# Performance work log

Hardware: AMD Instinct MI355X
Metric: run time of the kernel (lower is better)

Reference implementation:

```python
import math
import jax, jax.numpy as jnp
import numpy as np

TAU = 2.0
THR = 1.0
ALPHA = 10.0

T, B, IN_DIM, OUT_DIM = 64, 128, 2048, 2048


def setup_inputs() -> dict:
    key = jax.random.key(0)
    k1, k2, k3 = jax.random.split(key, 3)
    x_seq = jax.random.normal(k1, (T, B, IN_DIM), dtype=jnp.float32)
    # scale like nn.Linear default init so membrane potentials are O(1)
    W = jax.random.normal(k2, (OUT_DIM, IN_DIM), dtype=jnp.float32) / math.sqrt(IN_DIM)
    b = jax.random.normal(k3, (OUT_DIM,), dtype=jnp.float32) * 0.01
    return {"x_seq": x_seq, "W": W, "b": b}


def spike(x):
    # forward: hard threshold (surrogate gradient only matters in bwd)
    return (x > 0).astype(x.dtype)


def reference(x_seq, W, b):
    decay = math.exp(-1.0 / TAU)
    # hoist the linear layer out of the recurrence: one big GEMM
    cur_seq = jnp.einsum("tbi,oi->tbo", x_seq, W) + b  # (T, B, OUT_DIM)
    mem0 = jnp.zeros((x_seq.shape[1], W.shape[0]), dtype=x_seq.dtype)

    def step(mem, cur):
        mem = mem * decay + cur
        spk = spike(mem - THR)
        mem = mem - spk * THR
        return mem, spk

    _, spk_seq = jax.lax.scan(step, mem0, cur_seq)
    return spk_seq  # (T, B, OUT_DIM)
```

## Files before the change

kernel.cpp:

```cpp
#include <hip/hip_runtime.h>
#include <hip/hip_bf16.h>
#include <math.h>


typedef unsigned short u16;
typedef __attribute__((ext_vector_type(8))) short bf16x8;
typedef __attribute__((ext_vector_type(4))) float f32x4;

constexpr int T_STEPS = 64;
constexpr int BATCH   = 128;
constexpr int K_DIM   = 2048;
constexpr int N_DIM   = 2048;
constexpr int M_DIM   = T_STEPS * BATCH;
constexpr int NCHAIN  = BATCH * N_DIM;

constexpr float DECAY_F32 = (float)0.6065306597126334;
constexpr float BAND      = 2e-4f;

#define GLDS16(g, l) __builtin_amdgcn_global_load_lds(                       \
    (const __attribute__((address_space(1))) void*)(g),                      \
    (__attribute__((address_space(3))) void*)(l), 16, 0, 0)

__global__ __launch_bounds__(256)
void split_bf16(const float* __restrict__ X, const float* __restrict__ W,
                u16* __restrict__ Ah, u16* __restrict__ Al,
                u16* __restrict__ Wh, u16* __restrict__ Wl,
                unsigned int* __restrict__ counters) {
    if (blockIdx.x == 0 && threadIdx.x < 128) counters[threadIdx.x] = 0u;

    constexpr int NA8 = (M_DIM * K_DIM) / 8;
    constexpr int NW8 = (N_DIM * K_DIM) / 8;
    const int i = blockIdx.x * 256 + threadIdx.x;
    const float* src; u16* dh; u16* dl; int base;
    if (i < NA8)            { src = X; dh = Ah; dl = Al; base = i; }
    else if (i < NA8 + NW8) { src = W; dh = Wh; dl = Wl; base = i - NA8; }
    else return;

    const float4 v0 = *(const float4*)(src + (size_t)base * 8);
    const float4 v1 = *(const float4*)(src + (size_t)base * 8 + 4);
    const float f[8] = {v0.x, v0.y, v0.z, v0.w, v1.x, v1.y, v1.z, v1.w};
    unsigned int hp[4], lp[4];
#pragma unroll
    for (int q = 0; q < 8; q += 2) {
        u16 hh[2], ll[2];
#pragma unroll
        for (int e = 0; e < 2; e++) {
            __hip_bfloat16 hb = __float2bfloat16(f[q + e]);
            const float hf = __bfloat162float(hb);
            __hip_bfloat16 lb = __float2bfloat16(f[q + e] - hf);
            hh[e] = *(u16*)&hb;
            ll[e] = *(u16*)&lb;
        }
        hp[q >> 1] = (unsigned int)hh[0] | ((unsigned int)hh[1] << 16);
        lp[q >> 1] = (unsigned int)ll[0] | ((unsigned int)ll[1] << 16);
    }
    *(uint4*)(dh + (size_t)base * 8) = make_uint4(hp[0], hp[1], hp[2], hp[3]);
    *(uint4*)(dl + (size_t)base * 8) = make_uint4(lp[0], lp[1], lp[2], lp[3]);
}

__global__ __launch_bounds__(512, 2)
void gemm_bf16x3p(const u16* __restrict__ Ah, const u16* __restrict__ Al,
                  const u16* __restrict__ Bh, const u16* __restrict__ Bl,
                  const float* __restrict__ bias, float* __restrict__ C) {
    extern __shared__ __align__(16) u16 smem[];
    u16* const sAh = smem;
    u16* const sAl = smem + 3 * 8192;
    u16* const sBh = smem + 6 * 8192;
    u16* const sBl = smem + 6 * 8192 + 3 * 4096;

    const int tid  = threadIdx.x;
    const int orig = blockIdx.x + gridDim.x * blockIdx.y;
    const int wg   = (orig & 7) * 64 + (orig >> 3);
    const int m0   = (wg >> 4) * 256;
    const int n0   = (wg & 15) * 128;
    const int lane = tid & 63;
    const int wave = tid >> 6;
    const int wm   = wave >> 1;
    const int wn   = wave & 1;

    const int cA0 = tid, cA1 = tid + 512, cB0 = tid;
#define OFFA(c) ((size_t)(m0 + ((c) >> 6) * 16 + ((c) & 15)) * K_DIM + (((c) >> 4) & 3) * 8)
#define OFFB(c) ((size_t)(n0 + ((c) >> 6) * 16 + ((c) & 15)) * K_DIM + (((c) >> 4) & 3) * 8)
    const size_t a0 = OFFA(cA0), a1 = OFFA(cA1), b0 = OFFB(cB0);
#undef OFFA
#undef OFFB

    const int lA0 = wave * 512;
    const int lA1 = 4096 + wave * 512;
    const int lB0 = wave * 512;

    f32x4 acc[4][4];
#pragma unroll
    for (int i = 0; i < 4; i++)
#pragma unroll
        for (int j = 0; j < 4; j++) acc[i][j] = (f32x4){0.f, 0.f, 0.f, 0.f};

#define STAGE(s, kc) do {                                                    \
        const int kn_ = (kc) * 32;                                           \
        GLDS16(Ah + a0 + kn_, sAh + (s) * 8192 + lA0);                       \
        GLDS16(Ah + a1 + kn_, sAh + (s) * 8192 + lA1);                       \
        GLDS16(Al + a0 + kn_, sAl + (s) * 8192 + lA0);                       \
        GLDS16(Al + a1 + kn_, sAl + (s) * 8192 + lA1);                       \
        GLDS16(Bh + b0 + kn_, sBh + (s) * 4096 + lB0);                       \
        GLDS16(Bl + b0 + kn_, sBl + (s) * 4096 + lB0);                       \
    } while (0)

#define COMPUTE(rs) do {                                                     \
        bf16x8 fah[4], fal[4], fbh[4], fbl[4];                               \
        _Pragma("unroll")                                                    \
        for (int ti = 0; ti < 4; ti++) {                                     \
            const int ta = wm * 4 + ti;                                      \
            fah[ti] = *(const bf16x8*)&sAh[(rs) * 8192 + (ta * 64 + lane) * 8]; \
            fal[ti] = *(const bf16x8*)&sAl[(rs) * 8192 + (ta * 64 + lane) * 8]; \
        }                                                                    \
        _Pragma("unroll")                                                    \
        for (int tj = 0; tj < 4; tj++) {                                     \
            const int tb = wn * 4 + tj;                                      \
            fbh[tj] = *(const bf16x8*)&sBh[(rs) * 4096 + (tb * 64 + lane) * 8]; \
            fbl[tj] = *(const bf16x8*)&sBl[(rs) * 4096 + (tb * 64 + lane) * 8]; \
        }                                                                    \
        __builtin_amdgcn_s_setprio(1);                                       \
        _Pragma("unroll")                                                    \
        for (int ti = 0; ti < 4; ti++)                                       \
        _Pragma("unroll")                                                    \
        for (int tj = 0; tj < 4; tj++) {                                     \
            acc[ti][tj] = __builtin_amdgcn_mfma_f32_16x16x32_bf16(           \
                fah[ti], fbh[tj], acc[ti][tj], 0, 0, 0);                     \
            acc[ti][tj] = __builtin_amdgcn_mfma_f32_16x16x32_bf16(           \
                fah[ti], fbl[tj], acc[ti][tj], 0, 0, 0);                     \
            acc[ti][tj] = __builtin_amdgcn_mfma_f32_16x16x32_bf16(           \
                fal[ti], fbh[tj], acc[ti][tj], 0, 0, 0);                     \
        }                                                                    \
        __builtin_amdgcn_s_setprio(0);                                       \
    } while (0)

#define SYNC(vm) do {                                                        \
        asm volatile("s_waitcnt vmcnt(" #vm ")" ::: "memory");               \
        __builtin_amdgcn_sched_barrier(0);                                   \
        __builtin_amdgcn_s_barrier();                                        \
        __builtin_amdgcn_sched_barrier(0);                                   \
    } while (0)

    STAGE(0, 0);
    STAGE(1, 1);

    for (int kcb = 0; kcb < 63; kcb += 3) {
        SYNC(6);
        STAGE(2, kcb + 2);
        COMPUTE(0);
        SYNC(6);
        STAGE(0, kcb + 3);
        COMPUTE(1);
        SYNC(6);
        if (kcb + 4 < 64) STAGE(1, kcb + 4);
        COMPUTE(2);
    }
    SYNC(0);
    COMPUTE(0);

#undef SYNC
#undef COMPUTE
#undef STAGE

#pragma unroll
    for (int tj = 0; tj < 4; tj++) {
        const int n  = n0 + wn * 64 + tj * 16 + (lane & 15);
        const float bv = bias[n];
#pragma unroll
        for (int ti = 0; ti < 4; ti++) {
            const int mbase = m0 + wm * 64 + ti * 16 + (lane >> 4) * 4;
#pragma unroll
            for (int r = 0; r < 4; r++)
                C[(size_t)(mbase + r) * N_DIM + n] = acc[ti][tj][r] + bv;
        }
    }
}

__global__ __launch_bounds__(256)
void lif_scan_band4(float* __restrict__ buf, unsigned int* __restrict__ counters,
                    unsigned int* __restrict__ worklist) {
    const int idx = (blockIdx.x * 256 + threadIdx.x) * 4;
    float mem[4]  = {0.f, 0.f, 0.f, 0.f};
    bool  flag[4] = {false, false, false, false};
#pragma unroll
    for (int t = 0; t < T_STEPS; t++) {
        const size_t off = (size_t)t * NCHAIN + idx;
        const float4 v = *(const float4*)(buf + off);
        const float c[4] = {v.x, v.y, v.z, v.w};
        float s[4];
#pragma unroll
        for (int q = 0; q < 4; q++) {
            mem[q] = __fadd_rn(__fmul_rn(mem[q], DECAY_F32), c[q]);
            const float d = __fsub_rn(mem[q], 1.0f);
            const bool spk = d > 0.0f;
            if (fabsf(d) < BAND) flag[q] = true;
            s[q] = spk ? 1.0f : 0.0f;
            if (spk) mem[q] = __fsub_rn(mem[q], 1.0f);
        }
        *(float4*)(buf + off) = make_float4(s[0], s[1], s[2], s[3]);
    }
    const int b = idx >> 11;
#pragma unroll
    for (int q = 0; q < 4; q++) {
        if (flag[q]) {
            const unsigned int p = atomicAdd(&counters[b], 1u);
            worklist[b * 2048 + p] = (unsigned int)((idx + q) & 2047);
        }
    }
}

#define RG 16
#define RJ 4
#define BKR 64

__global__ __launch_bounds__(256)
void lif_repair2(const float* __restrict__ X, const float* __restrict__ W,
                 const float* __restrict__ bias,
                 const unsigned int* __restrict__ counters,
                 const unsigned int* __restrict__ worklist,
                 float* __restrict__ out) {
    __shared__ float sX[BKR][T_STEPS + 1];
    __shared__ float sW[RG][BKR + 1];
    __shared__ float scur[T_STEPS][RG + 1];
    __shared__ float sspk[T_STEPS][RG + 1];
    __shared__ int   so[RG];

    const int b = blockIdx.x / RJ;
    const int j = blockIdx.x % RJ;
    const unsigned int n_b = counters[b];
    if (n_b == 0) return;
    const int ngroups = (int)(n_b + RG - 1) / RG;

    const int tid = threadIdx.x;
    const int t   = tid & 63;
    const int oi  = tid >> 6;

    for (int g = j; g < ngroups; g += RJ) {
        if (tid < RG) {
            const int slot = g * RG + tid;
            so[tid] = (slot < (int)n_b) ? (int)worklist[b * 2048 + slot] : -1;
        }
        __syncthreads();

        float Csum[4] = {0.f, 0.f, 0.f, 0.f};
        float P[4]    = {0.f, 0.f, 0.f, 0.f};

        for (int c = 0; c < K_DIM / BKR; c++) {
            if (c > 0 && (c % 5) == 0) {
#pragma unroll
                for (int q = 0; q < 4; q++) {
                    Csum[q] = __fadd_rn(Csum[q], P[q]);
                    P[q] = 0.f;
                }
            }
            const int k0 = c * BKR;
            {
                const int ts = tid >> 2;
                const int kq = (tid & 3) * 16;
                const float* src = &X[(size_t)(ts * BATCH + b) * K_DIM + k0 + kq];
#pragma unroll
                for (int q = 0; q < 4; q++) {
                    const float4 v = *(const float4*)(src + q * 4);
                    sX[kq + q * 4 + 0][ts] = v.x;
                    sX[kq + q * 4 + 1][ts] = v.y;
                    sX[kq + q * 4 + 2][ts] = v.z;
                    sX[kq + q * 4 + 3][ts] = v.w;
                }
            }
            {
                const int wo  = tid >> 4;
                const int wkq = (tid & 15) * 4;
                const int o   = so[wo];
                float4 v = {0.f, 0.f, 0.f, 0.f};
                if (o >= 0) v = *(const float4*)&W[(size_t)o * K_DIM + k0 + wkq];
                sW[wo][wkq + 0] = v.x; sW[wo][wkq + 1] = v.y;
                sW[wo][wkq + 2] = v.z; sW[wo][wkq + 3] = v.w;
            }
            __syncthreads();
#pragma unroll 8
            for (int k = 0; k < BKR; k++) {
                const float xv = sX[k][t];
#pragma unroll
                for (int q = 0; q < 4; q++)
                    P[q] = fmaf(xv, sW[oi * 4 + q][k], P[q]);
            }
            __syncthreads();
        }
#pragma unroll
        for (int q = 0; q < 4; q++) {
            Csum[q] = __fadd_rn(Csum[q], P[q]);
            const int o = so[oi * 4 + q];
            scur[t][oi * 4 + q] = (o >= 0) ? __fadd_rn(Csum[q], bias[o]) : 0.f;
        }
        __syncthreads();
        if (tid < RG && so[tid] >= 0) {
            float mem = 0.0f;
            for (int tt = 0; tt < T_STEPS; tt++) {
                mem = __fadd_rn(__fmul_rn(mem, DECAY_F32), scur[tt][tid]);
                const float d = __fsub_rn(mem, 1.0f);
                const bool spk = d > 0.0f;
                sspk[tt][tid] = spk ? 1.0f : 0.0f;
                if (spk) mem = __fsub_rn(mem, 1.0f);
            }
        }
        __syncthreads();
#pragma unroll
        for (int q = 0; q < 4; q++) {
            const int o = so[oi * 4 + q];
            if (o >= 0)
                out[(size_t)t * NCHAIN + (size_t)b * N_DIM + o] = sspk[t][oi * 4 + q];
        }
        __syncthreads();
    }
}

__global__ __launch_bounds__(256)
void lif_openblas_q320(const float* __restrict__ X, const float* __restrict__ W,
                       const float* __restrict__ bias, float* __restrict__ out) {
    __shared__ float As[16][T_STEPS + 4];
    __shared__ float Ws[16][64 + 4];
    __shared__ float curbuf[T_STEPS][64 + 1];
    const int tid = threadIdx.x;
    const int o0 = blockIdx.x * 64, b0 = blockIdx.y;
    const int tm = (tid & 15) * 4, tn = (tid >> 4) * 4;
    float Csum[4][4], Pacc[4][4];
#pragma unroll
    for (int i = 0; i < 4; i++)
#pragma unroll
        for (int j = 0; j < 4; j++) { Csum[i][j] = 0.f; Pacc[i][j] = 0.f; }
    for (int c = 0; c < K_DIM / 16; c++) {
        if (c > 0 && (c % 20) == 0) {
#pragma unroll
            for (int i = 0; i < 4; i++)
#pragma unroll
                for (int j = 0; j < 4; j++) {
                    Csum[i][j] = __fadd_rn(Csum[i][j], Pacc[i][j]);
                    Pacc[i][j] = 0.f;
                }
        }
        const int k0 = c * 16;
        {
            const int t = tid >> 2, kq = (tid & 3) * 4;
            const float4 av = *(const float4*)&X[(size_t)(t * BATCH + b0) * K_DIM + k0 + kq];
            As[kq + 0][t] = av.x; As[kq + 1][t] = av.y;
            As[kq + 2][t] = av.z; As[kq + 3][t] = av.w;
            const float4 wv = *(const float4*)&W[(size_t)(o0 + t) * K_DIM + k0 + kq];
            Ws[kq + 0][t] = wv.x; Ws[kq + 1][t] = wv.y;
            Ws[kq + 2][t] = wv.z; Ws[kq + 3][t] = wv.w;
        }
        __syncthreads();
#pragma unroll
        for (int k = 0; k < 16; k++) {
            float a[4], w[4];
#pragma unroll
            for (int i = 0; i < 4; i++) a[i] = As[k][tm + i];
#pragma unroll
            for (int j = 0; j < 4; j++) w[j] = Ws[k][tn + j];
#pragma unroll
            for (int i = 0; i < 4; i++)
#pragma unroll
                for (int j = 0; j < 4; j++) Pacc[i][j] = fmaf(a[i], w[j], Pacc[i][j]);
        }
        __syncthreads();
    }
#pragma unroll
    for (int i = 0; i < 4; i++)
#pragma unroll
        for (int j = 0; j < 4; j++)
            curbuf[tm + i][tn + j] =
                __fadd_rn(__fadd_rn(Csum[i][j], Pacc[i][j]), bias[o0 + tn + j]);
    __syncthreads();
    if (tid < 64) {
        float mem = 0.0f;
#pragma unroll
        for (int t = 0; t < T_STEPS; t++) {
            mem = __fadd_rn(__fmul_rn(mem, DECAY_F32), curbuf[t][tid]);
            const float d = __fsub_rn(mem, 1.0f);
            const bool spk = d > 0.0f;
            out[(size_t)t * NCHAIN + (size_t)b0 * N_DIM + o0 + tid] = spk ? 1.0f : 0.0f;
            if (spk) mem = __fsub_rn(mem, 1.0f);
        }
    }
}

extern "C" void kernel_launch(void* const* d_in, const int* in_sizes, int n_in,
                              void* d_out, int out_size, void* d_ws, size_t ws_size,
                              hipStream_t stream) {
    const float* x = nullptr; const float* W = nullptr; const float* bias = nullptr;
    for (int i = 0; i < n_in; i++) {
        if      (in_sizes[i] == M_DIM * K_DIM) x    = (const float*)d_in[i];
        else if (in_sizes[i] == N_DIM * K_DIM) W    = (const float*)d_in[i];
        else if (in_sizes[i] == N_DIM)         bias = (const float*)d_in[i];
    }
    if (!x)    x    = (const float*)d_in[0];
    if (!W)    W    = (const float*)d_in[1];
    if (!bias) bias = (const float*)d_in[2];
    float* out = (float*)d_out;

    const size_t off_cnt = 0;
    const size_t off_wl  = 512;
    const size_t off_Ah  = off_wl + (size_t)128 * 2048 * 4;
    const size_t szA     = (size_t)M_DIM * K_DIM * 2;
    const size_t szW     = (size_t)N_DIM * K_DIM * 2;
    const size_t off_Al  = off_Ah + szA;
    const size_t off_Wh  = off_Al + szA;
    const size_t off_Wl  = off_Wh + szW;
    const size_t need    = off_Wl + szW;

    if (ws_size < need) {
        dim3 grid(N_DIM / 64, BATCH);
        lif_openblas_q320<<<grid, 256, 0, stream>>>(x, W, bias, out);
        return;
    }

    char* ws = (char*)d_ws;
    unsigned int* counters = (unsigned int*)(ws + off_cnt);
    unsigned int* worklist = (unsigned int*)(ws + off_wl);
    u16* Ah = (u16*)(ws + off_Ah);
    u16* Al = (u16*)(ws + off_Al);
    u16* Wh = (u16*)(ws + off_Wh);
    u16* Wl = (u16*)(ws + off_Wl);

    split_bf16<<<(M_DIM * K_DIM / 8 + N_DIM * K_DIM / 8) / 256, 256, 0, stream>>>(
        x, W, Ah, Al, Wh, Wl, counters);
    dim3 ggrid(N_DIM / 128, M_DIM / 256);
    gemm_bf16x3p<<<ggrid, 512, 147456, stream>>>(Ah, Al, Wh, Wl, bias, out);
    lif_scan_band4<<<NCHAIN / 1024, 256, 0, stream>>>(out, counters, worklist);
    lif_repair2<<<128 * RJ, 256, 0, stream>>>(x, W, bias, counters, worklist, out);
}
```

Before: 456.9 us.

## Fuse fp32-to-bf16 hi/lo split into GEMM load path, drop split kernel

Removes the separate split_bf16 pre-pass and instead has the GEMM load fp32 X and W tiles into registers, split them into bf16 high/low parts in-kernel, and write them to LDS. The LDS ring goes from three stages to two, and the counter reset moves into the GEMM kernel. This avoids writing and re-reading the bf16 copies of X and W through global memory and saves one kernel launch. In exchange, the GEMM now reads twice the bytes per tile, loses the asynchronous global-to-LDS path, and spends ALU time and registers on the conversion. That may reduce overlap with the MFMA work.

```diff
diff --git a/kernel.cpp b/kernel.cpp
--- a/kernel.cpp
+++ b/kernel.cpp
@@ -17,59 +17,20 @@
 constexpr float DECAY_F32 = (float)0.6065306597126334;
 constexpr float BAND      = 2e-4f;
 
-#define GLDS16(g, l) __builtin_amdgcn_global_load_lds(                       \
-    (const __attribute__((address_space(1))) void*)(g),                      \
-    (__attribute__((address_space(3))) void*)(l), 16, 0, 0)
-
-__global__ __launch_bounds__(256)
-void split_bf16(const float* __restrict__ X, const float* __restrict__ W,
-                u16* __restrict__ Ah, u16* __restrict__ Al,
-                u16* __restrict__ Wh, u16* __restrict__ Wl,
-                unsigned int* __restrict__ counters) {
-    if (blockIdx.x == 0 && threadIdx.x < 128) counters[threadIdx.x] = 0u;
-
-    constexpr int NA8 = (M_DIM * K_DIM) / 8;
-    constexpr int NW8 = (N_DIM * K_DIM) / 8;
-    const int i = blockIdx.x * 256 + threadIdx.x;
-    const float* src; u16* dh; u16* dl; int base;
-    if (i < NA8)            { src = X; dh = Ah; dl = Al; base = i; }
-    else if (i < NA8 + NW8) { src = W; dh = Wh; dl = Wl; base = i - NA8; }
-    else return;
-
-    const float4 v0 = *(const float4*)(src + (size_t)base * 8);
-    const float4 v1 = *(const float4*)(src + (size_t)base * 8 + 4);
-    const float f[8] = {v0.x, v0.y, v0.z, v0.w, v1.x, v1.y, v1.z, v1.w};
-    unsigned int hp[4], lp[4];
-#pragma unroll
-    for (int q = 0; q < 8; q += 2) {
-        u16 hh[2], ll[2];
-#pragma unroll
-        for (int e = 0; e < 2; e++) {
-            __hip_bfloat16 hb = __float2bfloat16(f[q + e]);
-            const float hf = __bfloat162float(hb);
-            __hip_bfloat16 lb = __float2bfloat16(f[q + e] - hf);
-            hh[e] = *(u16*)&hb;
-            ll[e] = *(u16*)&lb;
-        }
-        hp[q >> 1] = (unsigned int)hh[0] | ((unsigned int)hh[1] << 16);
-        lp[q >> 1] = (unsigned int)ll[0] | ((unsigned int)ll[1] << 16);
-    }
-    *(uint4*)(dh + (size_t)base * 8) = make_uint4(hp[0], hp[1], hp[2], hp[3]);
-    *(uint4*)(dl + (size_t)base * 8) = make_uint4(lp[0], lp[1], lp[2], lp[3]);
-}
-
 __global__ __launch_bounds__(512, 2)
-void gemm_bf16x3p(const u16* __restrict__ Ah, const u16* __restrict__ Al,
-                  const u16* __restrict__ Bh, const u16* __restrict__ Bl,
-                  const float* __restrict__ bias, float* __restrict__ C) {
+void gemm_bf16x3f(const float* __restrict__ X, const float* __restrict__ W,
+                  const float* __restrict__ bias, float* __restrict__ C,
+                  unsigned int* __restrict__ counters) {
     extern __shared__ __align__(16) u16 smem[];
     u16* const sAh = smem;
-    u16* const sAl = smem + 3 * 8192;
-    u16* const sBh = smem + 6 * 8192;
-    u16* const sBl = smem + 6 * 8192 + 3 * 4096;
+    u16* const sAl = smem + 2 * 8192;
+    u16* const sBh = smem + 4 * 8192;
+    u16* const sBl = smem + 4 * 8192 + 2 * 4096;
 
     const int tid  = threadIdx.x;
     const int orig = blockIdx.x + gridDim.x * blockIdx.y;
+    if (orig == 0 && tid < 128) counters[tid] = 0u;
+
     const int wg   = (orig & 7) * 64 + (orig >> 3);
     const int m0   = (wg >> 4) * 256;
     const int n0   = (wg & 15) * 128;
@@ -78,16 +39,14 @@
     const int wm   = wave >> 1;
     const int wn   = wave & 1;
 
-    const int cA0 = tid, cA1 = tid + 512, cB0 = tid;
-#define OFFA(c) ((size_t)(m0 + ((c) >> 6) * 16 + ((c) & 15)) * K_DIM + (((c) >> 4) & 3) * 8)
-#define OFFB(c) ((size_t)(n0 + ((c) >> 6) * 16 + ((c) & 15)) * K_DIM + (((c) >> 4) & 3) * 8)
-    const size_t a0 = OFFA(cA0), a1 = OFFA(cA1), b0 = OFFB(cB0);
-#undef OFFA
-#undef OFFB
-
-    const int lA0 = wave * 512;
-    const int lA1 = 4096 + wave * 512;
-    const int lB0 = wave * 512;
+    const int row_e = (tid >> 6) * 16 + (tid & 15);
+    const int ks_e  = ((tid >> 4) & 3) * 8;
+    const size_t a0f = (size_t)(m0 + row_e) * K_DIM + ks_e;
+    const size_t a1f = (size_t)(m0 + 128 + row_e) * K_DIM + ks_e;
+    const size_t b0f = (size_t)(n0 + row_e) * K_DIM + ks_e;
+    const int wA0 = tid * 8;
+    const int wA1 = 4096 + tid * 8;
+    const int wB0 = tid * 8;
 
     f32x4 acc[4][4];
 #pragma unroll
@@ -95,14 +54,50 @@
 #pragma unroll
         for (int j = 0; j < 4; j++) acc[i][j] = (f32x4){0.f, 0.f, 0.f, 0.f};
 
-#define STAGE(s, kc) do {                                                    \
-        const int kn_ = (kc) * 32;                                           \
-        GLDS16(Ah + a0 + kn_, sAh + (s) * 8192 + lA0);                       \
-        GLDS16(Ah + a1 + kn_, sAh + (s) * 8192 + lA1);                       \
-        GLDS16(Al + a0 + kn_, sAl + (s) * 8192 + lA0);                       \
-        GLDS16(Al + a1 + kn_, sAl + (s) * 8192 + lA1);                       \
-        GLDS16(Bh + b0 + kn_, sBh + (s) * 4096 + lB0);                       \
-        GLDS16(Bl + b0 + kn_, sBl + (s) * 4096 + lB0);                       \
+    float4 g0[6], g1[6];
+
+#define GLOAD(SET, kc) do {                                                  \
+        const size_t k_ = (size_t)(kc) * 32;                                 \
+        g##SET[0] = *(const float4*)(X + a0f + k_);                          \
+        g##SET[1] = *(const float4*)(X + a0f + k_ + 4);                      \
+        g##SET[2] = *(const float4*)(X + a1f + k_);                          \
+        g##SET[3] = *(const float4*)(X + a1f + k_ + 4);                      \
+        g##SET[4] = *(const float4*)(W + b0f + k_);                          \
+        g##SET[5] = *(const float4*)(W + b0f + k_ + 4);                      \
+    } while (0)
+
+#define DEK8(v0, v1, HI, LO) do {                                            \
+        const float f_[8] = {v0.x, v0.y, v0.z, v0.w, v1.x, v1.y, v1.z, v1.w};\
+        unsigned int hp_[4], lp_[4];                                         \
+        _Pragma("unroll")                                                    \
+        for (int q_ = 0; q_ < 8; q_ += 2) {                                  \
+            u16 hh_[2], ll_[2];                                              \
+            _Pragma("unroll")                                                \
+            for (int e_ = 0; e_ < 2; e_++) {                                 \
+                __hip_bfloat16 hb_ = __float2bfloat16(f_[q_ + e_]);          \
+                const float hf_ = __bfloat162float(hb_);                     \
+                __hip_bfloat16 lb_ = __float2bfloat16(f_[q_ + e_] - hf_);    \
+                hh_[e_] = *(u16*)&hb_;                                       \
+                ll_[e_] = *(u16*)&lb_;                                       \
+            }                                                                \
+            hp_[q_ >> 1] = (unsigned int)hh_[0] | ((unsigned int)hh_[1] << 16); \
+            lp_[q_ >> 1] = (unsigned int)ll_[0] | ((unsigned int)ll_[1] << 16); \
+        }                                                                    \
+        HI = make_uint4(hp_[0], hp_[1], hp_[2], hp_[3]);                     \
+        LO = make_uint4(lp_[0], lp_[1], lp_[2], lp_[3]);                     \
+    } while (0)
+
+#define CONVWRITE(s, SET) do {                                               \
+        uint4 hA0_, lA0_, hA1_, lA1_, hB_, lB_;                              \
+        DEK8(g##SET[0], g##SET[1], hA0_, lA0_);                              \
+        DEK8(g##SET[2], g##SET[3], hA1_, lA1_);                              \
+        DEK8(g##SET[4], g##SET[5], hB_, lB_);                                \
+        *(uint4*)&sAh[(s) * 8192 + wA0] = hA0_;                              \
+        *(uint4*)&sAl[(s) * 8192 + wA0] = lA0_;                              \
+        *(uint4*)&sAh[(s) * 8192 + wA1] = hA1_;                              \
+        *(uint4*)&sAl[(s) * 8192 + wA1] = lA1_;                              \
+        *(uint4*)&sBh[(s) * 4096 + wB0] = hB_;                               \
+        *(uint4*)&sBl[(s) * 4096 + wB0] = lB_;                               \
     } while (0)
 
 #define COMPUTE(rs) do {                                                     \
@@ -134,33 +129,67 @@
         __builtin_amdgcn_s_setprio(0);                                       \
     } while (0)
 
-#define SYNC(vm) do {                                                        \
-        asm volatile("s_waitcnt vmcnt(" #vm ")" ::: "memory");               \
+#define BAR do {                                                             \
         __builtin_amdgcn_sched_barrier(0);                                   \
         __builtin_amdgcn_s_barrier();                                        \
         __builtin_amdgcn_sched_barrier(0);                                   \
     } while (0)
-
-    STAGE(0, 0);
-    STAGE(1, 1);
-
-    for (int kcb = 0; kcb < 63; kcb += 3) {
-        SYNC(6);
-        STAGE(2, kcb + 2);
+#define VMW(n) do {                                                          \
+        asm volatile("s_waitcnt vmcnt(" #n ")" ::: "memory");                \
+        __builtin_amdgcn_sched_barrier(0);                                   \
+    } while (0)
+#define LGKM0 do {                                                           \
+        asm volatile("s_waitcnt lgkmcnt(0)" ::: "memory");                   \
+        __builtin_amdgcn_sched_barrier(0);                                   \
+    } while (0)
+
+    GLOAD(0, 0);
+    VMW(0);
+    CONVWRITE(0, 0);
+    GLOAD(1, 1);
+    LGKM0;
+
+    for (int kc = 0; kc < 60; kc += 2) {
+        BAR;
+        GLOAD(0, kc + 2);
+        VMW(6);
+        CONVWRITE(1, 1);
+        LGKM0;
         COMPUTE(0);
-        SYNC(6);
-        STAGE(0, kcb + 3);
+        BAR;
+        GLOAD(1, kc + 3);
+        VMW(6);
+        CONVWRITE(0, 0);
+        LGKM0;
         COMPUTE(1);
-        SYNC(6);
-        if (kcb + 4 < 64) STAGE(1, kcb + 4);
-        COMPUTE(2);
-    }
-    SYNC(0);
+    }
+    BAR;
+    GLOAD(0, 62);
+    VMW(6);
+    CONVWRITE(1, 1);
+    LGKM0;
     COMPUTE(0);
-
-#undef SYNC
+    BAR;
+    GLOAD(1, 63);
+    VMW(6);
+    CONVWRITE(0, 0);
+    LGKM0;
+    COMPUTE(1);
+    BAR;
+    VMW(0);
+    CONVWRITE(1, 1);
+    LGKM0;
+    COMPUTE(0);
+    BAR;
+    COMPUTE(1);
+
+#undef LGKM0
+#undef VMW
+#undef BAR
 #undef COMPUTE
-#undef STAGE
+#undef CONVWRITE
+#undef DEK8
+#undef GLOAD
 
 #pragma unroll
     for (int tj = 0; tj < 4; tj++) {
@@ -399,13 +428,7 @@
 
     const size_t off_cnt = 0;
     const size_t off_wl  = 512;
-    const size_t off_Ah  = off_wl + (size_t)128 * 2048 * 4;
-    const size_t szA     = (size_t)M_DIM * K_DIM * 2;
-    const size_t szW     = (size_t)N_DIM * K_DIM * 2;
-    const size_t off_Al  = off_Ah + szA;
-    const size_t off_Wh  = off_Al + szA;
-    const size_t off_Wl  = off_Wh + szW;
-    const size_t need    = off_Wl + szW;
+    const size_t need    = off_wl + (size_t)128 * 2048 * 4;
 
     if (ws_size < need) {
         dim3 grid(N_DIM / 64, BATCH);
@@ -416,15 +439,9 @@
     char* ws = (char*)d_ws;
     unsigned int* counters = (unsigned int*)(ws + off_cnt);
     unsigned int* worklist = (unsigned int*)(ws + off_wl);
-    u16* Ah = (u16*)(ws + off_Ah);
-    u16* Al = (u16*)(ws + off_Al);
-    u16* Wh = (u16*)(ws + off_Wh);
-    u16* Wl = (u16*)(ws + off_Wl);
-
-    split_bf16<<<(M_DIM * K_DIM / 8 + N_DIM * K_DIM / 8) / 256, 256, 0, stream>>>(
-        x, W, Ah, Al, Wh, Wl, counters);
+
     dim3 ggrid(N_DIM / 128, M_DIM / 256);
-    gemm_bf16x3p<<<ggrid, 512, 147456, stream>>>(Ah, Al, Wh, Wl, bias, out);
+    gemm_bf16x3f<<<ggrid, 512, 98304, stream>>>(x, W, bias, out, counters);
     lif_scan_band4<<<NCHAIN / 1024, 256, 0, stream>>>(out, counters, worklist);
     lif_repair2<<<128 * RJ, 256, 0, stream>>>(x, W, bias, counters, worklist, out);
 }
```

Result: faster. 444.0 us (-2.8%).
